# Performance work log

Measured on AMD Instinct MI355X. Metric: run time of the kernel, lower is better.

## Reference

```python
import jax, jax.numpy as jnp
import numpy as np

EMB = 1024
HEADS = 16
HEAD_DIM = EMB // HEADS


def setup_inputs() -> dict:
    key = jax.random.key(0)
    ks = jax.random.split(key, 5)
    x = jax.random.normal(ks[0], (2, 2048, EMB), dtype=jnp.float32)
    # per-head projection params, stacked over heads: [H, E, D]
    Wq = jax.random.normal(ks[1], (HEADS, EMB, HEAD_DIM), dtype=jnp.float32)
    Wk = jax.random.normal(ks[2], (HEADS, EMB, HEAD_DIM), dtype=jnp.float32)
    Wv = jax.random.normal(ks[3], (HEADS, EMB, HEAD_DIM), dtype=jnp.float32)
    # output projection (torch Linear weight [out, in], bias=False)
    Wo = jax.random.normal(ks[4], (EMB, EMB), dtype=jnp.float32) * (1.0 / np.sqrt(EMB))
    return {"x": x, "Wq": Wq, "Wk": Wk, "Wv": Wv, "Wo": Wo}


def reference(x, Wq, Wk, Wv, Wo):
    B, T, E = x.shape
    # per-head projections: [B, H, T, D]
    q = jnp.einsum('bte,hed->bhtd', x, Wq)
    k = jnp.einsum('bte,hed->bhtd', x, Wk)
    v = jnp.einsum('bte,hed->bhtd', x, Wv)
    scale = 1.0 / jnp.sqrt(jnp.asarray(HEAD_DIM, dtype=x.dtype))
    scores = jnp.einsum('bhtd,bhsd->bhts', q, k) * scale  # [B,H,T,T]
    s = jax.nn.softmax(scores, axis=-1)
    out = jnp.einsum('bhts,bhsd->bhtd', s, v)
    # concat heads along last dim in head order: [B, T, H*D]
    combined = jnp.transpose(out, (0, 2, 1, 3)).reshape(B, T, E)
    # residual + output projection (Linear bias=False: y = combined @ Wo.T)
    return x + combined @ Wo.T
```

## Files before the change

kernel.cpp:

```cpp
#include <hip/hip_runtime.h>

#define EMB   1024
#define HEADS 16
#define HDIM  64
#define BATCH 2
#define SEQ   2048
#define MROWS (BATCH*SEQ)
#define STR   40
#define QSCALE 0.1803368801111204f

typedef __attribute__((ext_vector_type(8))) short bf16x8;
typedef __attribute__((ext_vector_type(4))) float f32x4;
typedef unsigned short u16;

__device__ __forceinline__ u16 f2bf(float f) {
    unsigned u = __float_as_uint(f);
    u += 0x7fffu + ((u >> 16) & 1u);
    return (u16)(u >> 16);
}
__device__ __forceinline__ float bf2f(u16 h) {
    return __uint_as_float((unsigned)h << 16);
}
__device__ __forceinline__ float fast_exp2(float x) {
#if __has_builtin(__builtin_amdgcn_exp2f)
    return __builtin_amdgcn_exp2f(x);
#else
    return __expf(x * 0.6931471805599453f);
#endif
}
__device__ __forceinline__ unsigned pk_trunc(float lo, float hi) {
    return __builtin_amdgcn_perm(__float_as_uint(hi), __float_as_uint(lo),
                                 0x07060302u);
}

#define SWZ(r, ch) ((((r) << 6)) + ((((ch) ^ ((r) & 7))) << 3))

__global__ __launch_bounds__(256)
void prep1(const float* __restrict__ X, const float* __restrict__ Wq,
           const float* __restrict__ Wk, const float* __restrict__ Wv,
           u16* __restrict__ Xh, u16* __restrict__ Xl,
           u16* __restrict__ Qth, u16* __restrict__ Qtl,
           u16* __restrict__ Kth, u16* __restrict__ Ktl,
           u16* __restrict__ Vth)
{
    const int bx = blockIdx.x;
    if (bx < 2048) {
        int i = (bx * 256 + threadIdx.x) * 8;
#pragma unroll
        for (int half = 0; half < 2; ++half) {
            float4 v = *(const float4*)(X + i + half * 4);
            ushort4 hi, lo;
            hi.x = f2bf(v.x); lo.x = f2bf(v.x - bf2f(hi.x));
            hi.y = f2bf(v.y); lo.y = f2bf(v.y - bf2f(hi.y));
            hi.z = f2bf(v.z); lo.z = f2bf(v.z - bf2f(hi.z));
            hi.w = f2bf(v.w); lo.w = f2bf(v.w - bf2f(hi.w));
            *(ushort4*)(Xh + i + half * 4) = hi;
            *(ushort4*)(Xl + i + half * 4) = lo;
        }
    } else if (bx < 3072) {
        const int f = bx - 2048;
        const int z = f >> 9, y = (f >> 5) & 15, x = f & 31;
        const float* W  = z ? Wk  : Wq;
        u16* Oh         = z ? Kth : Qth;
        u16* Ol         = z ? Ktl : Qtl;
        const int d  = threadIdx.x & 63;
        const int e0 = (x * 4 + (threadIdx.x >> 6)) * 8;
        const float* src = W + ((size_t)y * EMB + e0) * HDIM + d;
        ushort4 h0, h1, l0, l1;
        float v; u16 hv;
        v = src[0 * 64]; hv = f2bf(v); h0.x = hv; l0.x = f2bf(v - bf2f(hv));
        v = src[1 * 64]; hv = f2bf(v); h0.y = hv; l0.y = f2bf(v - bf2f(hv));
        v = src[2 * 64]; hv = f2bf(v); h0.z = hv; l0.z = f2bf(v - bf2f(hv));
        v = src[3 * 64]; hv = f2bf(v); h0.w = hv; l0.w = f2bf(v - bf2f(hv));
        v = src[4 * 64]; hv = f2bf(v); h1.x = hv; l1.x = f2bf(v - bf2f(hv));
        v = src[5 * 64]; hv = f2bf(v); h1.y = hv; l1.y = f2bf(v - bf2f(hv));
        v = src[6 * 64]; hv = f2bf(v); h1.z = hv; l1.z = f2bf(v - bf2f(hv));
        v = src[7 * 64]; hv = f2bf(v); h1.w = hv; l1.w = f2bf(v - bf2f(hv));
        size_t obase = ((size_t)y * HDIM + d) * EMB + e0;
        *(ushort4*)(Oh + obase)     = h0;
        *(ushort4*)(Oh + obase + 4) = h1;
        *(ushort4*)(Ol + obase)     = l0;
        *(ushort4*)(Ol + obase + 4) = l1;
    } else {
        const int f = bx - 3072;
        const int y = f >> 5, x = f & 31;
        const int d  = threadIdx.x & 63;
        const int e0 = (x * 4 + (threadIdx.x >> 6)) * 8;
        const float* src = Wv + ((size_t)y * EMB + e0) * HDIM + d;
        ushort4 h0, h1;
        h0.x = f2bf(src[0 * 64]); h0.y = f2bf(src[1 * 64]);
        h0.z = f2bf(src[2 * 64]); h0.w = f2bf(src[3 * 64]);
        h1.x = f2bf(src[4 * 64]); h1.y = f2bf(src[5 * 64]);
        h1.z = f2bf(src[6 * 64]); h1.w = f2bf(src[7 * 64]);
        size_t obase = ((size_t)y * HDIM + d) * EMB + e0;
        *(ushort4*)(Vth + obase)     = h0;
        *(ushort4*)(Vth + obase + 4) = h1;
    }
}

__global__ __launch_bounds__(256, 2)
void qkv_fused(const u16* __restrict__ Xh, const u16* __restrict__ Xl,
               const u16* __restrict__ Wqh, const u16* __restrict__ Wql,
               const u16* __restrict__ Wkh, const u16* __restrict__ Wkl,
               const u16* __restrict__ Wvt,
               u16* __restrict__ Qh, u16* __restrict__ Ql,
               u16* __restrict__ Kh, u16* __restrict__ Kl,
               u16* __restrict__ Vt)
{
    const int z  = blockIdx.z;
    const bool isV = (z == 2);
    const int m0 = blockIdx.x * 128;
    const int n0 = blockIdx.y * 128;
    const int t    = threadIdx.x;
    const int wave = t >> 6, lane = t & 63;
    const int wm = wave & 1, wn = wave >> 1;
    const int l16 = lane & 15, quad = lane >> 4;

    __shared__ u16 Ahs[128][STR];
    __shared__ u16 Als[128][STR];
    __shared__ u16 Bhs[128][STR];
    __shared__ u16 Bls[128][STR];

    const u16* Bh_g = isV ? Wvt : (z ? Wkh : Wqh);
    const u16* Bl_g = z ? Wkl : Wql;

    const int ar0 = t >> 2, ak = (t & 3) * 8, ar1 = ar0 + 64;

    f32x4 acc[4][4];
#pragma unroll
    for (int i = 0; i < 4; ++i)
#pragma unroll
        for (int j = 0; j < 4; ++j) acc[i][j] = (f32x4){0.f, 0.f, 0.f, 0.f};

    bf16x8 cur[8], nxt[8], nx2[8];
#define QK_LOAD(dst, kk)                                                            \
    do {                                                                            \
        dst[0] = *(const bf16x8*)(Xh  + (size_t)(m0 + ar0) * EMB + (kk) + ak);      \
        dst[1] = *(const bf16x8*)(Xh  + (size_t)(m0 + ar1) * EMB + (kk) + ak);      \
        dst[4] = *(const bf16x8*)(Bh_g + (size_t)(n0 + ar0) * EMB + (kk) + ak);     \
        dst[5] = *(const bf16x8*)(Bh_g + (size_t)(n0 + ar1) * EMB + (kk) + ak);     \
        if (!isV) {                                                                 \
            dst[2] = *(const bf16x8*)(Xl  + (size_t)(m0 + ar0) * EMB + (kk) + ak);  \
            dst[3] = *(const bf16x8*)(Xl  + (size_t)(m0 + ar1) * EMB + (kk) + ak);  \
            dst[6] = *(const bf16x8*)(Bl_g + (size_t)(n0 + ar0) * EMB + (kk) + ak); \
            dst[7] = *(const bf16x8*)(Bl_g + (size_t)(n0 + ar1) * EMB + (kk) + ak); \
        }                                                                           \
    } while (0)

    QK_LOAD(cur, 0);
    QK_LOAD(nxt, 32);

    for (int k0 = 0; k0 < EMB; k0 += 32) {
        __syncthreads();
        *(bf16x8*)&Ahs[ar0][ak] = cur[0];  *(bf16x8*)&Ahs[ar1][ak] = cur[1];
        *(bf16x8*)&Bhs[ar0][ak] = cur[4];  *(bf16x8*)&Bhs[ar1][ak] = cur[5];
        if (!isV) {
            *(bf16x8*)&Als[ar0][ak] = cur[2];  *(bf16x8*)&Als[ar1][ak] = cur[3];
            *(bf16x8*)&Bls[ar0][ak] = cur[6];  *(bf16x8*)&Bls[ar1][ak] = cur[7];
        }
        __syncthreads();

        const int kn = (k0 + 64 < EMB) ? k0 + 64 : 0;
        QK_LOAD(nx2, kn);

        bf16x8 B4h[4], B4l[4];
#pragma unroll
        for (int j = 0; j < 4; ++j) {
            B4h[j] = *(const bf16x8*)&Bhs[wn * 64 + 16 * j + l16][quad * 8];
            if (!isV)
                B4l[j] = *(const bf16x8*)&Bls[wn * 64 + 16 * j + l16][quad * 8];
        }
#pragma unroll
        for (int i = 0; i < 4; ++i) {
            bf16x8 Ai_h = *(const bf16x8*)&Ahs[wm * 64 + 16 * i + l16][quad * 8];
            if (!isV) {
                bf16x8 Ai_l = *(const bf16x8*)&Als[wm * 64 + 16 * i + l16][quad * 8];
#pragma unroll
                for (int j = 0; j < 4; ++j) {
                    acc[i][j] = __builtin_amdgcn_mfma_f32_16x16x32_bf16(Ai_h, B4h[j], acc[i][j], 0, 0, 0);
                    acc[i][j] = __builtin_amdgcn_mfma_f32_16x16x32_bf16(Ai_h, B4l[j], acc[i][j], 0, 0, 0);
                    acc[i][j] = __builtin_amdgcn_mfma_f32_16x16x32_bf16(Ai_l, B4h[j], acc[i][j], 0, 0, 0);
                }
            } else {
#pragma unroll
                for (int j = 0; j < 4; ++j)
                    acc[i][j] = __builtin_amdgcn_mfma_f32_16x16x32_bf16(Ai_h, B4h[j], acc[i][j], 0, 0, 0);
            }
        }
#pragma unroll
        for (int q = 0; q < 8; ++q) { cur[q] = nxt[q]; nxt[q] = nx2[q]; }
    }
#undef QK_LOAD

    const int b = m0 >> 11;
    const int h = (n0 + wn * 64) >> 6;
    if (isV) {
#pragma unroll
        for (int i = 0; i < 4; ++i)
#pragma unroll
            for (int j = 0; j < 4; ++j) {
                int d  = 16 * j + l16;
                int tt = (m0 & (SEQ - 1)) + wm * 64 + 16 * i + quad * 4;
                ushort4 o;
                o.x = f2bf(acc[i][j][0]); o.y = f2bf(acc[i][j][1]);
                o.z = f2bf(acc[i][j][2]); o.w = f2bf(acc[i][j][3]);
                *(ushort4*)(Vt + ((size_t)(b * HEADS + h) * HDIM + d) * SEQ + tt) = o;
            }
    } else {
        u16* Oh = z ? Kh : Qh;
        u16* Ol = z ? Kl : Ql;
        const float esc = z ? 1.0f : QSCALE;
#pragma unroll
        for (int i = 0; i < 4; ++i)
#pragma unroll
            for (int r = 0; r < 4; ++r) {
                int tt = (m0 & (SEQ - 1)) + wm * 64 + 16 * i + quad * 4 + r;
                size_t rowbase = ((size_t)(b * HEADS + h) * SEQ + tt) * HDIM;
#pragma unroll
                for (int j = 0; j < 4; ++j) {
                    int d = 16 * j + l16;
                    float v = acc[i][j][r] * esc;
                    u16 hv = f2bf(v);
                    Oh[rowbase + d] = hv;
                    Ol[rowbase + d] = f2bf(v - bf2f(hv));
                }
            }
    }
}

__global__ __launch_bounds__(256, 4)
void attn_mfma(const u16* __restrict__ Qh, const u16* __restrict__ Ql,
               const u16* __restrict__ Kh, const u16* __restrict__ Kl,
               const u16* __restrict__ Vt, u16* __restrict__ Cb,
               const float* __restrict__ Wo, u16* __restrict__ Woh)
{
    const int w = blockIdx.x;
    if (w >= 1024) {
        int base = ((w - 1024) * 256 + threadIdx.x) * 8;
#pragma unroll 4
        for (int it = 0; it < 32; ++it) {
#pragma unroll
            for (int half = 0; half < 2; ++half) {
                float4 v = *(const float4*)(Wo + base + half * 4);
                ushort4 o;
                o.x = f2bf(v.x); o.y = f2bf(v.y); o.z = f2bf(v.z); o.w = f2bf(v.w);
                *(ushort4*)(Woh + base + half * 4) = o;
            }
            base += 16 * 256 * 8;
        }
        return;
    }

    const int g    = w >> 3;
    const int qt0  = (g & 31) * 64;
    const int bh   = (w & 7) + ((g >> 5) << 3);

    const int t    = threadIdx.x;
    const int wave = t >> 6;
    const int lane = t & 63;
    const int l16  = lane & 15;
    const int quad = lane >> 4;

    __shared__ u16 Ksh[4096];
    __shared__ u16 Ksl[4096];
    __shared__ u16 Vs [4096];
    __shared__ u16 Ps [4096];

    const size_t bh_off = (size_t)bh * SEQ * HDIM;
    const u16* Qhb = Qh + bh_off;
    const u16* Qlb = Ql + bh_off;
    const u16* Khb = Kh + bh_off;
    const u16* Klb = Kl + bh_off;
    const u16* Vtb = Vt + bh_off;

    const int qrow = qt0 + wave * 16 + l16;
    bf16x8 aQh[2], aQl[2];
    {
        const u16* bH = Qhb + (size_t)qrow * HDIM + quad * 8;
        const u16* bL = Qlb + (size_t)qrow * HDIM + quad * 8;
        aQh[0] = *(const bf16x8*)(bH);
        aQh[1] = *(const bf16x8*)(bH + 32);
        aQl[0] = *(const bf16x8*)(bL);
        aQl[1] = *(const bf16x8*)(bL + 32);
    }

    f32x4 accO[4];
    float m_i = -1e30f, l_i = 0.f;
#pragma unroll
    for (int j = 0; j < 4; ++j) accO[j] = (f32x4){0.f, 0.f, 0.f, 0.f};

    const int sr0 = t >> 3, sch = t & 7, sr1 = sr0 + 32;
    const int gc  = sch * 8;
    const int so0 = SWZ(sr0, sch), so1 = SWZ(sr1, sch);

    bf16x8 cur[6], nxt[6];
#define KV_LOAD(dst, ss)                                                       \
    do {                                                                       \
        dst[0] = *(const bf16x8*)(Khb + (size_t)((ss) + sr0) * HDIM + gc);     \
        dst[1] = *(const bf16x8*)(Khb + (size_t)((ss) + sr1) * HDIM + gc);     \
        dst[2] = *(const bf16x8*)(Klb + (size_t)((ss) + sr0) * HDIM + gc);     \
        dst[3] = *(const bf16x8*)(Klb + (size_t)((ss) + sr1) * HDIM + gc);     \
        dst[4] = *(const bf16x8*)(Vtb + (size_t)sr0 * SEQ + (ss) + gc);        \
        dst[5] = *(const bf16x8*)(Vtb + (size_t)sr1 * SEQ + (ss) + gc);        \
    } while (0)

    KV_LOAD(cur, 0);

    for (int s0 = 0; s0 < SEQ; s0 += 64) {
        __syncthreads();
        *(bf16x8*)&Ksh[so0] = cur[0];  *(bf16x8*)&Ksh[so1] = cur[1];
        *(bf16x8*)&Ksl[so0] = cur[2];  *(bf16x8*)&Ksl[so1] = cur[3];
        *(bf16x8*)&Vs [so0] = cur[4];  *(bf16x8*)&Vs [so1] = cur[5];
        __syncthreads();

        const int sn = (s0 + 64 < SEQ) ? s0 + 64 : 0;
        KV_LOAD(nxt, sn);

        f32x4 accS[4];
#pragma unroll
        for (int i = 0; i < 4; ++i) accS[i] = (f32x4){0.f, 0.f, 0.f, 0.f};
        __builtin_amdgcn_s_setprio(1);
#pragma unroll
        for (int c = 0; c < 2; ++c) {
#pragma unroll
            for (int i = 0; i < 4; ++i) {
                bf16x8 kh_ = *(const bf16x8*)&Ksh[SWZ(16 * i + l16, 4 * c + quad)];
                bf16x8 kl_ = *(const bf16x8*)&Ksl[SWZ(16 * i + l16, 4 * c + quad)];
                accS[i] = __builtin_amdgcn_mfma_f32_16x16x32_bf16(kh_, aQh[c], accS[i], 0, 0, 0);
                accS[i] = __builtin_amdgcn_mfma_f32_16x16x32_bf16(kl_, aQh[c], accS[i], 0, 0, 0);
                accS[i] = __builtin_amdgcn_mfma_f32_16x16x32_bf16(kh_, aQl[c], accS[i], 0, 0, 0);
            }
        }
        __builtin_amdgcn_s_setprio(0);

        {
            float vmax = fmaxf(fmaxf(accS[0][0], accS[0][1]),
                               fmaxf(accS[0][2], accS[0][3]));
#pragma unroll
            for (int i = 1; i < 4; ++i)
                vmax = fmaxf(vmax, fmaxf(fmaxf(accS[i][0], accS[i][1]),
                                         fmaxf(accS[i][2], accS[i][3])));
            vmax = fmaxf(vmax, __shfl_xor(vmax, 16, 64));
            vmax = fmaxf(vmax, __shfl_xor(vmax, 32, 64));
            float mn   = fmaxf(m_i, vmax);
            float alph = fast_exp2(m_i - mn);
            m_i = mn;
            float P[4][4], s = 0.f;
#pragma unroll
            for (int i = 0; i < 4; ++i)
#pragma unroll
                for (int r = 0; r < 4; ++r) {
                    P[i][r] = fast_exp2(accS[i][r] - mn);
                    s += P[i][r];
                }
            s += __shfl_xor(s, 16, 64);
            s += __shfl_xor(s, 32, 64);
            l_i = l_i * alph + s;
#pragma unroll
            for (int j = 0; j < 4; ++j) accO[j] *= alph;

            const int prow = wave * 16 + l16;
#pragma unroll
            for (int i = 0; i < 4; ++i) {
                uint2 pv;
                pv.x = pk_trunc(P[i][0], P[i][1]);
                pv.y = pk_trunc(P[i][2], P[i][3]);
                *(uint2*)&Ps[SWZ(prow, 2 * i + (quad >> 1)) + ((quad & 1) << 2)] = pv;
            }
        }

        __builtin_amdgcn_s_setprio(1);
#pragma unroll
        for (int c = 0; c < 2; ++c) {
            bf16x8 bP = *(const bf16x8*)&Ps[SWZ(wave * 16 + l16, 4 * c + quad)];
#pragma unroll
            for (int j = 0; j < 4; ++j) {
                bf16x8 aV = *(const bf16x8*)&Vs[SWZ(16 * j + l16, 4 * c + quad)];
                accO[j] = __builtin_amdgcn_mfma_f32_16x16x32_bf16(aV, bP, accO[j], 0, 0, 0);
            }
        }
        __builtin_amdgcn_s_setprio(0);
#pragma unroll
        for (int q = 0; q < 6; ++q) cur[q] = nxt[q];
    }
#undef KV_LOAD

    const int b = bh >> 4, h = bh & 15;
    {
        const int row = qt0 + wave * 16 + l16;
        const float inv = 1.f / l_i;
#pragma unroll
        for (int j = 0; j < 4; ++j) {
            ushort4 o;
            o.x = f2bf(accO[j][0] * inv); o.y = f2bf(accO[j][1] * inv);
            o.z = f2bf(accO[j][2] * inv); o.w = f2bf(accO[j][3] * inv);
            *(ushort4*)&Cb[((size_t)b * SEQ + row) * EMB + h * HDIM + 16 * j + quad * 4] = o;
        }
    }
}

__global__ __launch_bounds__(256, 2)
void oproj_mfma(const u16* __restrict__ Cb, const u16* __restrict__ Woh,
                const float* __restrict__ X, float* __restrict__ Y)
{
    const int m0 = blockIdx.x * 64;
    const int n0 = blockIdx.y * 128;
    const int t    = threadIdx.x;
    const int wave = t >> 6, lane = t & 63;
    const int wm = wave & 1, wn = wave >> 1;
    const int l16 = lane & 15, quad = lane >> 4;

    __shared__ u16 Ahs[64][STR];
    __shared__ u16 Bhs[128][STR];

    const int ar0 = t >> 2, ak = (t & 3) * 8, ar1 = ar0 + 64;

    f32x4 acc[2][4];
#pragma unroll
    for (int i = 0; i < 2; ++i)
#pragma unroll
        for (int j = 0; j < 4; ++j) acc[i][j] = (f32x4){0.f, 0.f, 0.f, 0.f};

    bf16x8 cur[3], nxt[3], nx2[3];
#define O_LOAD(dst, kk)                                                         \
    do {                                                                        \
        dst[0] = *(const bf16x8*)(Cb  + (size_t)(m0 + ar0) * EMB + (kk) + ak);  \
        dst[1] = *(const bf16x8*)(Woh + (size_t)(n0 + ar0) * EMB + (kk) + ak);  \
        dst[2] = *(const bf16x8*)(Woh + (size_t)(n0 + ar1) * EMB + (kk) + ak);  \
    } while (0)

    O_LOAD(cur, 0);
    O_LOAD(nxt, 32);

    for (int k0 = 0; k0 < EMB; k0 += 32) {
        __syncthreads();
        *(bf16x8*)&Ahs[ar0][ak] = cur[0];
        *(bf16x8*)&Bhs[ar0][ak] = cur[1];  *(bf16x8*)&Bhs[ar1][ak] = cur[2];
        __syncthreads();

        const int kn = (k0 + 64 < EMB) ? k0 + 64 : 0;
        O_LOAD(nx2, kn);

        bf16x8 B4[4];
#pragma unroll
        for (int j = 0; j < 4; ++j)
            B4[j] = *(const bf16x8*)&Bhs[wn * 64 + 16 * j + l16][quad * 8];
#pragma unroll
        for (int i = 0; i < 2; ++i) {
            bf16x8 Ai = *(const bf16x8*)&Ahs[wm * 32 + 16 * i + l16][quad * 8];
#pragma unroll
            for (int j = 0; j < 4; ++j)
                acc[i][j] = __builtin_amdgcn_mfma_f32_16x16x32_bf16(Ai, B4[j], acc[i][j], 0, 0, 0);
        }
#pragma unroll
        for (int q = 0; q < 3; ++q) { cur[q] = nxt[q]; nxt[q] = nx2[q]; }
    }
#undef O_LOAD

#pragma unroll
    for (int i = 0; i < 2; ++i)
#pragma unroll
        for (int r = 0; r < 4; ++r) {
            int m = m0 + wm * 32 + 16 * i + quad * 4 + r;
#pragma unroll
            for (int j = 0; j < 4; ++j) {
                int n = n0 + wn * 64 + 16 * j + l16;
                Y[(size_t)m * EMB + n] = acc[i][j][r] + X[(size_t)m * EMB + n];
            }
        }
}

extern "C" void kernel_launch(void* const* d_in, const int* in_sizes, int n_in,
                              void* d_out, int out_size, void* d_ws,
                              size_t ws_size, hipStream_t stream)
{
    const float* x  = (const float*)d_in[0];
    const float* Wq = (const float*)d_in[1];
    const float* Wk = (const float*)d_in[2];
    const float* Wv = (const float*)d_in[3];
    const float* Wo = (const float*)d_in[4];
    float* Y = (float*)d_out;

    const size_t NPER = (size_t)MROWS * EMB;
    u16* base  = (u16*)d_ws;
    u16* Qh    = base;
    u16* Ql    = Qh + NPER;
    u16* Kh    = Ql + NPER;
    u16* Kl    = Kh + NPER;
    u16* Vt    = Kl + NPER;
    u16* Xh    = Vt + NPER;
    u16* Xl    = Xh + NPER;
    u16* Wtq_h = Xl + NPER;
    u16* Wtq_l = Wtq_h + EMB * EMB;
    u16* Wtk_h = Wtq_l + EMB * EMB;
    u16* Wtk_l = Wtk_h + EMB * EMB;
    u16* Wvt   = (u16*)d_out;
    u16* Cb    = Xh;
    u16* Woh   = Xl;

    prep1<<<dim3(3584), 256, 0, stream>>>(x, Wq, Wk, Wv, Xh, Xl,
                                          Wtq_h, Wtq_l, Wtk_h, Wtk_l, Wvt);
    qkv_fused<<<dim3(32, 8, 3), 256, 0, stream>>>(Xh, Xl, Wtq_h, Wtq_l,
                                                  Wtk_h, Wtk_l, Wvt,
                                                  Qh, Ql, Kh, Kl, Vt);
    attn_mfma<<<dim3(1040), 256, 0, stream>>>(Qh, Ql, Kh, Kl, Vt, Cb, Wo, Woh);
    oproj_mfma<<<dim3(64, 8), 256, 0, stream>>>(Cb, Woh, x, Y);
}
```

Baseline: 268.9 us.

## Switch attention to 32x32x16 MFMA with 128-row query tiles and register-shuffled P

The attention kernel moves from 16x16x32 to 32x32x16 bf16 MFMA tiles. Each wave now owns 32 query rows and each block owns 128, which halves the grid and the K/V tile reloads per query. The probability matrix is passed from the score layout to the PV operand layout with cross-lane shuffles instead of an LDS round trip, so the Ps buffer goes away. The cost is more accumulator registers per lane, with launch bounds lowered to 2 blocks per SM, and only 512 attention blocks, which could reduce occupancy and hurt load balance.

```diff
diff --git a/kernel.cpp b/kernel.cpp
--- a/kernel.cpp
+++ b/kernel.cpp
@@ -11,6 +11,7 @@
 
 typedef __attribute__((ext_vector_type(8))) short bf16x8;
 typedef __attribute__((ext_vector_type(4))) float f32x4;
+typedef __attribute__((ext_vector_type(16))) float f32x16;
 typedef unsigned short u16;
 
 __device__ __forceinline__ u16 f2bf(float f) {
@@ -228,15 +229,15 @@
     }
 }
 
-__global__ __launch_bounds__(256, 4)
+__global__ __launch_bounds__(256, 2)
 void attn_mfma(const u16* __restrict__ Qh, const u16* __restrict__ Ql,
                const u16* __restrict__ Kh, const u16* __restrict__ Kl,
                const u16* __restrict__ Vt, u16* __restrict__ Cb,
                const float* __restrict__ Wo, u16* __restrict__ Woh)
 {
     const int w = blockIdx.x;
-    if (w >= 1024) {
-        int base = ((w - 1024) * 256 + threadIdx.x) * 8;
+    if (w >= 512) {
+        int base = ((w - 512) * 256 + threadIdx.x) * 8;
 #pragma unroll 4
         for (int it = 0; it < 32; ++it) {
 #pragma unroll
@@ -252,19 +253,18 @@
     }
 
     const int g    = w >> 3;
-    const int qt0  = (g & 31) * 64;
-    const int bh   = (w & 7) + ((g >> 5) << 3);
+    const int qt0  = (g & 15) * 128;
+    const int bh   = (w & 7) + ((g >> 4) << 3);
 
     const int t    = threadIdx.x;
     const int wave = t >> 6;
     const int lane = t & 63;
-    const int l16  = lane & 15;
-    const int quad = lane >> 4;
+    const int l31  = lane & 31;
+    const int hi   = lane >> 5;
 
     __shared__ u16 Ksh[4096];
     __shared__ u16 Ksl[4096];
     __shared__ u16 Vs [4096];
-    __shared__ u16 Ps [4096];
 
     const size_t bh_off = (size_t)bh * SEQ * HDIM;
     const u16* Qhb = Qh + bh_off;
@@ -273,21 +273,23 @@
     const u16* Klb = Kl + bh_off;
     const u16* Vtb = Vt + bh_off;
 
-    const int qrow = qt0 + wave * 16 + l16;
-    bf16x8 aQh[2], aQl[2];
-    {
-        const u16* bH = Qhb + (size_t)qrow * HDIM + quad * 8;
-        const u16* bL = Qlb + (size_t)qrow * HDIM + quad * 8;
-        aQh[0] = *(const bf16x8*)(bH);
-        aQh[1] = *(const bf16x8*)(bH + 32);
-        aQl[0] = *(const bf16x8*)(bL);
-        aQl[1] = *(const bf16x8*)(bL + 32);
-    }
-
-    f32x4 accO[4];
+    const int qw0 = qt0 + wave * 32;
+
+    bf16x8 bQh[4], bQl[4];
+#pragma unroll
+    for (int ks = 0; ks < 4; ++ks) {
+        const u16* pH = Qhb + (size_t)(qw0 + l31) * HDIM + ks * 16 + hi * 8;
+        const u16* pL = Qlb + (size_t)(qw0 + l31) * HDIM + ks * 16 + hi * 8;
+        bQh[ks] = *(const bf16x8*)pH;
+        bQl[ks] = *(const bf16x8*)pL;
+    }
+
+    f32x16 accO[2];
+#pragma unroll
+    for (int dt = 0; dt < 2; ++dt)
+#pragma unroll
+        for (int r = 0; r < 16; ++r) accO[dt][r] = 0.f;
     float m_i = -1e30f, l_i = 0.f;
-#pragma unroll
-    for (int j = 0; j < 4; ++j) accO[j] = (f32x4){0.f, 0.f, 0.f, 0.f};
 
     const int sr0 = t >> 3, sch = t & 7, sr1 = sr0 + 32;
     const int gc  = sch * 8;
@@ -316,68 +318,93 @@
         const int sn = (s0 + 64 < SEQ) ? s0 + 64 : 0;
         KV_LOAD(nxt, sn);
 
-        f32x4 accS[4];
-#pragma unroll
-        for (int i = 0; i < 4; ++i) accS[i] = (f32x4){0.f, 0.f, 0.f, 0.f};
+        f32x16 accS[2];
+#pragma unroll
+        for (int kt = 0; kt < 2; ++kt)
+#pragma unroll
+            for (int r = 0; r < 16; ++r) accS[kt][r] = 0.f;
         __builtin_amdgcn_s_setprio(1);
 #pragma unroll
-        for (int c = 0; c < 2; ++c) {
-#pragma unroll
-            for (int i = 0; i < 4; ++i) {
-                bf16x8 kh_ = *(const bf16x8*)&Ksh[SWZ(16 * i + l16, 4 * c + quad)];
-                bf16x8 kl_ = *(const bf16x8*)&Ksl[SWZ(16 * i + l16, 4 * c + quad)];
-                accS[i] = __builtin_amdgcn_mfma_f32_16x16x32_bf16(kh_, aQh[c], accS[i], 0, 0, 0);
-                accS[i] = __builtin_amdgcn_mfma_f32_16x16x32_bf16(kl_, aQh[c], accS[i], 0, 0, 0);
-                accS[i] = __builtin_amdgcn_mfma_f32_16x16x32_bf16(kh_, aQl[c], accS[i], 0, 0, 0);
-            }
+        for (int ks = 0; ks < 4; ++ks) {
+            bf16x8 kh0 = *(const bf16x8*)&Ksh[SWZ(l31,      2 * ks + hi)];
+            bf16x8 kh1 = *(const bf16x8*)&Ksh[SWZ(32 + l31, 2 * ks + hi)];
+            bf16x8 kl0 = *(const bf16x8*)&Ksl[SWZ(l31,      2 * ks + hi)];
+            bf16x8 kl1 = *(const bf16x8*)&Ksl[SWZ(32 + l31, 2 * ks + hi)];
+            accS[0] = __builtin_amdgcn_mfma_f32_32x32x16_bf16(kh0, bQh[ks], accS[0], 0, 0, 0);
+            accS[1] = __builtin_amdgcn_mfma_f32_32x32x16_bf16(kh1, bQh[ks], accS[1], 0, 0, 0);
+            accS[0] = __builtin_amdgcn_mfma_f32_32x32x16_bf16(kl0, bQh[ks], accS[0], 0, 0, 0);
+            accS[1] = __builtin_amdgcn_mfma_f32_32x32x16_bf16(kl1, bQh[ks], accS[1], 0, 0, 0);
+            accS[0] = __builtin_amdgcn_mfma_f32_32x32x16_bf16(kh0, bQl[ks], accS[0], 0, 0, 0);
+            accS[1] = __builtin_amdgcn_mfma_f32_32x32x16_bf16(kh1, bQl[ks], accS[1], 0, 0, 0);
         }
         __builtin_amdgcn_s_setprio(0);
 
+        float P[2][16];
         {
-            float vmax = fmaxf(fmaxf(accS[0][0], accS[0][1]),
-                               fmaxf(accS[0][2], accS[0][3]));
-#pragma unroll
-            for (int i = 1; i < 4; ++i)
-                vmax = fmaxf(vmax, fmaxf(fmaxf(accS[i][0], accS[i][1]),
-                                         fmaxf(accS[i][2], accS[i][3])));
-            vmax = fmaxf(vmax, __shfl_xor(vmax, 16, 64));
+            float vmax = accS[0][0];
+#pragma unroll
+            for (int r = 1; r < 16; ++r) vmax = fmaxf(vmax, accS[0][r]);
+#pragma unroll
+            for (int r = 0; r < 16; ++r) vmax = fmaxf(vmax, accS[1][r]);
             vmax = fmaxf(vmax, __shfl_xor(vmax, 32, 64));
             float mn   = fmaxf(m_i, vmax);
             float alph = fast_exp2(m_i - mn);
             m_i = mn;
-            float P[4][4], s = 0.f;
-#pragma unroll
-            for (int i = 0; i < 4; ++i)
-#pragma unroll
-                for (int r = 0; r < 4; ++r) {
-                    P[i][r] = fast_exp2(accS[i][r] - mn);
-                    s += P[i][r];
+            float s = 0.f;
+#pragma unroll
+            for (int kt = 0; kt < 2; ++kt)
+#pragma unroll
+                for (int r = 0; r < 16; ++r) {
+                    P[kt][r] = fast_exp2(accS[kt][r] - mn);
+                    s += P[kt][r];
                 }
-            s += __shfl_xor(s, 16, 64);
             s += __shfl_xor(s, 32, 64);
             l_i = l_i * alph + s;
 #pragma unroll
-            for (int j = 0; j < 4; ++j) accO[j] *= alph;
-
-            const int prow = wave * 16 + l16;
-#pragma unroll
-            for (int i = 0; i < 4; ++i) {
-                uint2 pv;
-                pv.x = pk_trunc(P[i][0], P[i][1]);
-                pv.y = pk_trunc(P[i][2], P[i][3]);
-                *(uint2*)&Ps[SWZ(prow, 2 * i + (quad >> 1)) + ((quad & 1) << 2)] = pv;
+            for (int dt = 0; dt < 2; ++dt)
+#pragma unroll
+                for (int r = 0; r < 16; ++r) accO[dt][r] *= alph;
+        }
+
+        unsigned pp[2][4][2];
+#pragma unroll
+        for (int kt = 0; kt < 2; ++kt)
+#pragma unroll
+            for (int rq = 0; rq < 4; ++rq) {
+                pp[kt][rq][0] = pk_trunc(P[kt][4 * rq + 0], P[kt][4 * rq + 1]);
+                pp[kt][rq][1] = pk_trunc(P[kt][4 * rq + 2], P[kt][4 * rq + 3]);
             }
+        unsigned rcv[2][2][2];
+#pragma unroll
+        for (int kt = 0; kt < 2; ++kt)
+#pragma unroll
+            for (int m = 0; m < 2; ++m)
+#pragma unroll
+                for (int u = 0; u < 2; ++u) {
+                    unsigned snd = hi ? pp[kt][2 * m][u] : pp[kt][2 * m + 1][u];
+                    rcv[kt][m][u] = __shfl_xor(snd, 32, 64);
+                }
+        bf16x8 bP[4];
+#pragma unroll
+        for (int ks = 0; ks < 4; ++ks) {
+            const int kt = ks >> 1, m = ks & 1;
+            unsigned a0 = pp[kt][2 * m + hi][0], a1 = pp[kt][2 * m + hi][1];
+            unsigned b0 = rcv[kt][m][0],         b1 = rcv[kt][m][1];
+            union { unsigned u[4]; bf16x8 v; } tmp;
+            tmp.u[0] = hi ? b0 : a0;
+            tmp.u[1] = hi ? b1 : a1;
+            tmp.u[2] = hi ? a0 : b0;
+            tmp.u[3] = hi ? a1 : b1;
+            bP[ks] = tmp.v;
         }
 
         __builtin_amdgcn_s_setprio(1);
 #pragma unroll
-        for (int c = 0; c < 2; ++c) {
-            bf16x8 bP = *(const bf16x8*)&Ps[SWZ(wave * 16 + l16, 4 * c + quad)];
-#pragma unroll
-            for (int j = 0; j < 4; ++j) {
-                bf16x8 aV = *(const bf16x8*)&Vs[SWZ(16 * j + l16, 4 * c + quad)];
-                accO[j] = __builtin_amdgcn_mfma_f32_16x16x32_bf16(aV, bP, accO[j], 0, 0, 0);
-            }
+        for (int ks = 0; ks < 4; ++ks) {
+            bf16x8 aV0 = *(const bf16x8*)&Vs[SWZ(l31,      2 * ks + hi)];
+            bf16x8 aV1 = *(const bf16x8*)&Vs[SWZ(32 + l31, 2 * ks + hi)];
+            accO[0] = __builtin_amdgcn_mfma_f32_32x32x16_bf16(aV0, bP[ks], accO[0], 0, 0, 0);
+            accO[1] = __builtin_amdgcn_mfma_f32_32x32x16_bf16(aV1, bP[ks], accO[1], 0, 0, 0);
         }
         __builtin_amdgcn_s_setprio(0);
 #pragma unroll
@@ -386,17 +413,21 @@
 #undef KV_LOAD
 
     const int b = bh >> 4, h = bh & 15;
-    {
-        const int row = qt0 + wave * 16 + l16;
-        const float inv = 1.f / l_i;
-#pragma unroll
-        for (int j = 0; j < 4; ++j) {
+    const int qrow = qw0 + l31;
+    const float inv = 1.f / l_i;
+    u16* crow = Cb + ((size_t)b * SEQ + qrow) * EMB + h * HDIM;
+#pragma unroll
+    for (int dt = 0; dt < 2; ++dt)
+#pragma unroll
+        for (int rq = 0; rq < 4; ++rq) {
+            const int d0 = dt * 32 + 8 * rq + 4 * hi;
             ushort4 o;
-            o.x = f2bf(accO[j][0] * inv); o.y = f2bf(accO[j][1] * inv);
-            o.z = f2bf(accO[j][2] * inv); o.w = f2bf(accO[j][3] * inv);
-            *(ushort4*)&Cb[((size_t)b * SEQ + row) * EMB + h * HDIM + 16 * j + quad * 4] = o;
-        }
-    }
+            o.x = f2bf(accO[dt][4 * rq + 0] * inv);
+            o.y = f2bf(accO[dt][4 * rq + 1] * inv);
+            o.z = f2bf(accO[dt][4 * rq + 2] * inv);
+            o.w = f2bf(accO[dt][4 * rq + 3] * inv);
+            *(ushort4*)(crow + d0) = o;
+        }
 }
 
 __global__ __launch_bounds__(256, 2)
@@ -503,6 +534,6 @@
     qkv_fused<<<dim3(32, 8, 3), 256, 0, stream>>>(Xh, Xl, Wtq_h, Wtq_l,
                                                   Wtk_h, Wtk_l, Wvt,
                                                   Qh, Ql, Kh, Kl, Vt);
-    attn_mfma<<<dim3(1040), 256, 0, stream>>>(Qh, Ql, Kh, Kl, Vt, Cb, Wo, Woh);
+    attn_mfma<<<dim3(528), 256, 0, stream>>>(Qh, Ql, Kh, Kl, Vt, Cb, Wo, Woh);
     oproj_mfma<<<dim3(64, 8), 256, 0, stream>>>(Cb, Woh, x, Y);
 }
```

New measurement: 277.7 us. 1.03x slower.

## Restructure attention to 32x32 MFMA with split-K waves and direct-to-LDS loads

Applied to the files above, without the earlier changes.

Rewrites the attention kernel to use 32x32x16 bf16 MFMAs. Waves are split into two query halves times two key halves, and the two key-half partial softmax states are merged through LDS at the end. K/V tiles are double-buffered via global_load_lds straight into LDS, with one barrier per iteration instead of two. The P matrix is passed between MFMAs through lane shuffles rather than LDS, and a lazy rescale skips the accumulator correction when the running max grows by at most 8. The larger LDS footprint lowers occupancy to 3 blocks, and the lazy-max threshold risks exp2 overflow margins.

```diff
diff --git a/kernel.cpp b/kernel.cpp
--- a/kernel.cpp
+++ b/kernel.cpp
@@ -11,6 +11,7 @@
 
 typedef __attribute__((ext_vector_type(8))) short bf16x8;
 typedef __attribute__((ext_vector_type(4))) float f32x4;
+typedef __attribute__((ext_vector_type(16))) float f32x16;
 typedef unsigned short u16;
 
 __device__ __forceinline__ u16 f2bf(float f) {
@@ -31,6 +32,11 @@
 __device__ __forceinline__ unsigned pk_trunc(float lo, float hi) {
     return __builtin_amdgcn_perm(__float_as_uint(hi), __float_as_uint(lo),
                                  0x07060302u);
+}
+__device__ __forceinline__ void gload16(const u16* g, u16* l) {
+    __builtin_amdgcn_global_load_lds(
+        (const __attribute__((address_space(1))) unsigned int*)g,
+        (__attribute__((address_space(3))) unsigned int*)l, 16, 0, 0);
 }
 
 #define SWZ(r, ch) ((((r) << 6)) + ((((ch) ^ ((r) & 7))) << 3))
@@ -228,7 +234,7 @@
     }
 }
 
-__global__ __launch_bounds__(256, 4)
+__global__ __launch_bounds__(256, 3)
 void attn_mfma(const u16* __restrict__ Qh, const u16* __restrict__ Ql,
                const u16* __restrict__ Kh, const u16* __restrict__ Kl,
                const u16* __restrict__ Vt, u16* __restrict__ Cb,
@@ -251,20 +257,19 @@
         return;
     }
 
-    const int g    = w >> 3;
-    const int qt0  = (g & 31) * 64;
-    const int bh   = (w & 7) + ((g >> 5) << 3);
+    const int g     = w >> 3;
+    const int qtile = g & 31;
+    const int bh    = (w & 7) + ((g >> 5) << 3);
 
     const int t    = threadIdx.x;
     const int wave = t >> 6;
     const int lane = t & 63;
-    const int l16  = lane & 15;
-    const int quad = lane >> 4;
-
-    __shared__ u16 Ksh[4096];
-    __shared__ u16 Ksl[4096];
-    __shared__ u16 Vs [4096];
-    __shared__ u16 Ps [4096];
+    const int l31  = lane & 31;
+    const int hi   = lane >> 5;
+    const int wq   = wave & 1;
+    const int wk   = wave >> 1;
+
+    __shared__ u16 lds[24576];
 
     const size_t bh_off = (size_t)bh * SEQ * HDIM;
     const u16* Qhb = Qh + bh_off;
@@ -273,128 +278,166 @@
     const u16* Klb = Kl + bh_off;
     const u16* Vtb = Vt + bh_off;
 
-    const int qrow = qt0 + wave * 16 + l16;
-    bf16x8 aQh[2], aQl[2];
-    {
-        const u16* bH = Qhb + (size_t)qrow * HDIM + quad * 8;
-        const u16* bL = Qlb + (size_t)qrow * HDIM + quad * 8;
-        aQh[0] = *(const bf16x8*)(bH);
-        aQh[1] = *(const bf16x8*)(bH + 32);
-        aQl[0] = *(const bf16x8*)(bL);
-        aQl[1] = *(const bf16x8*)(bL + 32);
-    }
-
-    f32x4 accO[4];
+    const int qb0 = qtile * 64 + wq * 32;
+
+    bf16x8 bQh[4], bQl[4];
+#pragma unroll
+    for (int ks = 0; ks < 4; ++ks) {
+        const u16* pH = Qhb + (size_t)(qb0 + l31) * HDIM + ks * 16 + hi * 8;
+        const u16* pL = Qlb + (size_t)(qb0 + l31) * HDIM + ks * 16 + hi * 8;
+        bQh[ks] = *(const bf16x8*)pH;
+        bQl[ks] = *(const bf16x8*)pL;
+    }
+
+    f32x16 accO0, accO1;
+#pragma unroll
+    for (int r = 0; r < 16; ++r) { accO0[r] = 0.f; accO1[r] = 0.f; }
     float m_i = -1e30f, l_i = 0.f;
-#pragma unroll
-    for (int j = 0; j < 4; ++j) accO[j] = (f32x4){0.f, 0.f, 0.f, 0.f};
-
-    const int sr0 = t >> 3, sch = t & 7, sr1 = sr0 + 32;
-    const int gc  = sch * 8;
-    const int so0 = SWZ(sr0, sch), so1 = SWZ(sr1, sch);
-
-    bf16x8 cur[6], nxt[6];
-#define KV_LOAD(dst, ss)                                                       \
-    do {                                                                       \
-        dst[0] = *(const bf16x8*)(Khb + (size_t)((ss) + sr0) * HDIM + gc);     \
-        dst[1] = *(const bf16x8*)(Khb + (size_t)((ss) + sr1) * HDIM + gc);     \
-        dst[2] = *(const bf16x8*)(Klb + (size_t)((ss) + sr0) * HDIM + gc);     \
-        dst[3] = *(const bf16x8*)(Klb + (size_t)((ss) + sr1) * HDIM + gc);     \
-        dst[4] = *(const bf16x8*)(Vtb + (size_t)sr0 * SEQ + (ss) + gc);        \
-        dst[5] = *(const bf16x8*)(Vtb + (size_t)sr1 * SEQ + (ss) + gc);        \
+
+    const int r8  = lane >> 3;
+    const int cSw = (lane & 7) ^ (r8 & 7);
+    const int rowA = wave * 16 + r8;
+    const size_t koffA = (size_t)rowA * HDIM + cSw * 8;
+    const size_t koffB = koffA + 8 * HDIM;
+    const size_t voffA = (size_t)rowA * SEQ + cSw * 8;
+    const size_t voffB = voffA + (size_t)8 * SEQ;
+
+#define STAGE(b, s0_)                                                              \
+    do { const int bb = (b) * 12288; const int wb = bb + wave * 1024;              \
+        gload16(Khb + (size_t)(s0_) * HDIM + koffA, &lds[wb]);                     \
+        gload16(Khb + (size_t)(s0_) * HDIM + koffB, &lds[wb + 512]);               \
+        gload16(Klb + (size_t)(s0_) * HDIM + koffA, &lds[wb + 4096]);              \
+        gload16(Klb + (size_t)(s0_) * HDIM + koffB, &lds[wb + 4096 + 512]);        \
+        gload16(Vtb + (s0_) + voffA,                &lds[wb + 8192]);              \
+        gload16(Vtb + (s0_) + voffB,                &lds[wb + 8192 + 512]);        \
     } while (0)
 
-    KV_LOAD(cur, 0);
-
-    for (int s0 = 0; s0 < SEQ; s0 += 64) {
+    STAGE(0, 0);
+    __syncthreads();
+
+    const int l7 = lane & 7;
+    for (int it = 0; it < 32; ++it) {
+        const int cur = it & 1;
+        if (it < 31) STAGE(cur ^ 1, (it + 1) * 64);
+
+        const u16* KhL = &lds[cur * 12288];
+        const u16* KlL = KhL + 4096;
+        const u16* VL  = KhL + 8192;
+
+        f32x16 accS;
+#pragma unroll
+        for (int r = 0; r < 16; ++r) accS[r] = 0.f;
+        __builtin_amdgcn_s_setprio(1);
+#pragma unroll
+        for (int ks = 0; ks < 4; ++ks) {
+            const int off = (wk * 32 + l31) * 64 + (((2 * ks + hi) ^ l7)) * 8;
+            bf16x8 kh = *(const bf16x8*)(KhL + off);
+            bf16x8 kl = *(const bf16x8*)(KlL + off);
+            accS = __builtin_amdgcn_mfma_f32_32x32x16_bf16(kh, bQh[ks], accS, 0, 0, 0);
+            accS = __builtin_amdgcn_mfma_f32_32x32x16_bf16(kl, bQh[ks], accS, 0, 0, 0);
+            accS = __builtin_amdgcn_mfma_f32_32x32x16_bf16(kh, bQl[ks], accS, 0, 0, 0);
+        }
+        __builtin_amdgcn_s_setprio(0);
+
+        float P[16];
+        {
+            float vmax = fmaxf(fmaxf(accS[0], accS[1]), fmaxf(accS[2], accS[3]));
+#pragma unroll
+            for (int r = 4; r < 16; r += 4)
+                vmax = fmaxf(vmax, fmaxf(fmaxf(accS[r], accS[r + 1]),
+                                         fmaxf(accS[r + 2], accS[r + 3])));
+            vmax = fmaxf(vmax, __shfl_xor(vmax, 32, 64));
+            if (!__all(vmax - m_i <= 8.0f)) {
+                float mn = fmaxf(m_i, vmax);
+                float alph = fast_exp2(m_i - mn);
+                m_i = mn;
+                l_i *= alph;
+#pragma unroll
+                for (int r = 0; r < 16; ++r) { accO0[r] *= alph; accO1[r] *= alph; }
+            }
+            float s = 0.f;
+#pragma unroll
+            for (int r = 0; r < 16; ++r) {
+                P[r] = fast_exp2(accS[r] - m_i);
+                s += P[r];
+            }
+            s += __shfl_xor(s, 32, 64);
+            l_i += s;
+        }
+
+        unsigned A_[4], B_[4];
+#pragma unroll
+        for (int rq = 0; rq < 4; ++rq) {
+            A_[rq] = pk_trunc(P[4 * rq + 0], P[4 * rq + 1]);
+            B_[rq] = pk_trunc(P[4 * rq + 2], P[4 * rq + 3]);
+        }
+        bf16x8 bP[2];
+#pragma unroll
+        for (int ks = 0; ks < 2; ++ks) {
+            unsigned sndA = hi ? A_[2 * ks] : A_[2 * ks + 1];
+            unsigned sndB = hi ? B_[2 * ks] : B_[2 * ks + 1];
+            unsigned rcvA = __shfl_xor(sndA, 32, 64);
+            unsigned rcvB = __shfl_xor(sndB, 32, 64);
+            union { unsigned u[4]; bf16x8 v; } tmp;
+            tmp.u[0] = hi ? rcvA : A_[2 * ks];
+            tmp.u[1] = hi ? rcvB : B_[2 * ks];
+            tmp.u[2] = hi ? A_[2 * ks + 1] : rcvA;
+            tmp.u[3] = hi ? B_[2 * ks + 1] : rcvB;
+            bP[ks] = tmp.v;
+        }
+
+        __builtin_amdgcn_s_setprio(1);
+#pragma unroll
+        for (int ks = 0; ks < 2; ++ks) {
+            const int c0 = (4 * wk + 2 * ks + hi);
+            bf16x8 v0 = *(const bf16x8*)(VL + l31 * 64        + ((c0 ^ l7)) * 8);
+            bf16x8 v1 = *(const bf16x8*)(VL + (32 + l31) * 64 + ((c0 ^ l7)) * 8);
+            accO0 = __builtin_amdgcn_mfma_f32_32x32x16_bf16(v0, bP[ks], accO0, 0, 0, 0);
+            accO1 = __builtin_amdgcn_mfma_f32_32x32x16_bf16(v1, bP[ks], accO1, 0, 0, 0);
+        }
+        __builtin_amdgcn_s_setprio(0);
+
         __syncthreads();
-        *(bf16x8*)&Ksh[so0] = cur[0];  *(bf16x8*)&Ksh[so1] = cur[1];
-        *(bf16x8*)&Ksl[so0] = cur[2];  *(bf16x8*)&Ksl[so1] = cur[3];
-        *(bf16x8*)&Vs [so0] = cur[4];  *(bf16x8*)&Vs [so1] = cur[5];
-        __syncthreads();
-
-        const int sn = (s0 + 64 < SEQ) ? s0 + 64 : 0;
-        KV_LOAD(nxt, sn);
-
-        f32x4 accS[4];
-#pragma unroll
-        for (int i = 0; i < 4; ++i) accS[i] = (f32x4){0.f, 0.f, 0.f, 0.f};
-        __builtin_amdgcn_s_setprio(1);
-#pragma unroll
-        for (int c = 0; c < 2; ++c) {
-#pragma unroll
-            for (int i = 0; i < 4; ++i) {
-                bf16x8 kh_ = *(const bf16x8*)&Ksh[SWZ(16 * i + l16, 4 * c + quad)];
-                bf16x8 kl_ = *(const bf16x8*)&Ksl[SWZ(16 * i + l16, 4 * c + quad)];
-                accS[i] = __builtin_amdgcn_mfma_f32_16x16x32_bf16(kh_, aQh[c], accS[i], 0, 0, 0);
-                accS[i] = __builtin_amdgcn_mfma_f32_16x16x32_bf16(kl_, aQh[c], accS[i], 0, 0, 0);
-                accS[i] = __builtin_amdgcn_mfma_f32_16x16x32_bf16(kh_, aQl[c], accS[i], 0, 0, 0);
-            }
-        }
-        __builtin_amdgcn_s_setprio(0);
-
-        {
-            float vmax = fmaxf(fmaxf(accS[0][0], accS[0][1]),
-                               fmaxf(accS[0][2], accS[0][3]));
-#pragma unroll
-            for (int i = 1; i < 4; ++i)
-                vmax = fmaxf(vmax, fmaxf(fmaxf(accS[i][0], accS[i][1]),
-                                         fmaxf(accS[i][2], accS[i][3])));
-            vmax = fmaxf(vmax, __shfl_xor(vmax, 16, 64));
-            vmax = fmaxf(vmax, __shfl_xor(vmax, 32, 64));
-            float mn   = fmaxf(m_i, vmax);
-            float alph = fast_exp2(m_i - mn);
-            m_i = mn;
-            float P[4][4], s = 0.f;
-#pragma unroll
-            for (int i = 0; i < 4; ++i)
-#pragma unroll
-                for (int r = 0; r < 4; ++r) {
-                    P[i][r] = fast_exp2(accS[i][r] - mn);
-                    s += P[i][r];
-                }
-            s += __shfl_xor(s, 16, 64);
-            s += __shfl_xor(s, 32, 64);
-            l_i = l_i * alph + s;
-#pragma unroll
-            for (int j = 0; j < 4; ++j) accO[j] *= alph;
-
-            const int prow = wave * 16 + l16;
-#pragma unroll
-            for (int i = 0; i < 4; ++i) {
-                uint2 pv;
-                pv.x = pk_trunc(P[i][0], P[i][1]);
-                pv.y = pk_trunc(P[i][2], P[i][3]);
-                *(uint2*)&Ps[SWZ(prow, 2 * i + (quad >> 1)) + ((quad & 1) << 2)] = pv;
-            }
-        }
-
-        __builtin_amdgcn_s_setprio(1);
-#pragma unroll
-        for (int c = 0; c < 2; ++c) {
-            bf16x8 bP = *(const bf16x8*)&Ps[SWZ(wave * 16 + l16, 4 * c + quad)];
-#pragma unroll
-            for (int j = 0; j < 4; ++j) {
-                bf16x8 aV = *(const bf16x8*)&Vs[SWZ(16 * j + l16, 4 * c + quad)];
-                accO[j] = __builtin_amdgcn_mfma_f32_16x16x32_bf16(aV, bP, accO[j], 0, 0, 0);
-            }
-        }
-        __builtin_amdgcn_s_setprio(0);
-#pragma unroll
-        for (int q = 0; q < 6; ++q) cur[q] = nxt[q];
-    }
-#undef KV_LOAD
-
-    const int b = bh >> 4, h = bh & 15;
-    {
-        const int row = qt0 + wave * 16 + l16;
-        const float inv = 1.f / l_i;
-#pragma unroll
-        for (int j = 0; j < 4; ++j) {
+    }
+#undef STAGE
+
+    float* fb = (float*)lds;
+    const int slot = (wave * 64 + lane) * 34;
+#pragma unroll
+    for (int r = 0; r < 16; ++r) {
+        fb[slot + r]      = accO0[r];
+        fb[slot + 16 + r] = accO1[r];
+    }
+    fb[slot + 32] = m_i;
+    fb[slot + 33] = l_i;
+    __syncthreads();
+    if (wk == 0) {
+        const int ps = ((wave + 2) * 64 + lane) * 34;
+        const float m1 = fb[ps + 32], l1 = fb[ps + 33];
+        const float mS = fmaxf(m_i, m1);
+        float f0 = fast_exp2(m_i - mS);
+        float f1 = fast_exp2(m1 - mS);
+        const float inv = 1.f / (l_i * f0 + l1 * f1);
+        f0 *= inv; f1 *= inv;
+        const int b = bh >> 4, h = bh & 15;
+        u16* crow = Cb + ((size_t)b * SEQ + qb0 + l31) * EMB + h * HDIM;
+#pragma unroll
+        for (int rq = 0; rq < 4; ++rq) {
             ushort4 o;
-            o.x = f2bf(accO[j][0] * inv); o.y = f2bf(accO[j][1] * inv);
-            o.z = f2bf(accO[j][2] * inv); o.w = f2bf(accO[j][3] * inv);
-            *(ushort4*)&Cb[((size_t)b * SEQ + row) * EMB + h * HDIM + 16 * j + quad * 4] = o;
+            o.x = f2bf(accO0[4 * rq + 0] * f0 + fb[ps + 4 * rq + 0] * f1);
+            o.y = f2bf(accO0[4 * rq + 1] * f0 + fb[ps + 4 * rq + 1] * f1);
+            o.z = f2bf(accO0[4 * rq + 2] * f0 + fb[ps + 4 * rq + 2] * f1);
+            o.w = f2bf(accO0[4 * rq + 3] * f0 + fb[ps + 4 * rq + 3] * f1);
+            *(ushort4*)(crow + 8 * rq + 4 * hi) = o;
+        }
+#pragma unroll
+        for (int rq = 0; rq < 4; ++rq) {
+            ushort4 o;
+            o.x = f2bf(accO1[4 * rq + 0] * f0 + fb[ps + 16 + 4 * rq + 0] * f1);
+            o.y = f2bf(accO1[4 * rq + 1] * f0 + fb[ps + 16 + 4 * rq + 1] * f1);
+            o.z = f2bf(accO1[4 * rq + 2] * f0 + fb[ps + 16 + 4 * rq + 2] * f1);
+            o.w = f2bf(accO1[4 * rq + 3] * f0 + fb[ps + 16 + 4 * rq + 3] * f1);
+            *(ushort4*)(crow + 32 + 8 * rq + 4 * hi) = o;
         }
     }
 }
```

Result: slower. 282.2 us (+5.0%).

## Stage QKV GEMM tiles with direct global-to-LDS loads and double buffering

Applied to the files above, without the earlier changes.

The QKV projection GEMM stops staging tiles through registers. Tiles now go straight into a double-buffered LDS array with global_load_lds, and the two barriers per k-step become one. This frees the VGPRs that held the three prefetch stages and removes the LDS write instructions. In exchange the rows are unpadded (stride 32, no swizzle), so the MFMA fragment reads may hit LDS bank conflicts, and prefetch depth drops from two steps to one.

```diff
diff --git a/kernel.cpp b/kernel.cpp
--- a/kernel.cpp
+++ b/kernel.cpp
@@ -31,6 +31,11 @@
 __device__ __forceinline__ unsigned pk_trunc(float lo, float hi) {
     return __builtin_amdgcn_perm(__float_as_uint(hi), __float_as_uint(lo),
                                  0x07060302u);
+}
+__device__ __forceinline__ void gload16(const u16* g, u16* l) {
+    __builtin_amdgcn_global_load_lds(
+        (const __attribute__((address_space(1))) unsigned int*)g,
+        (__attribute__((address_space(3))) unsigned int*)l, 16, 0, 0);
 }
 
 #define SWZ(r, ch) ((((r) << 6)) + ((((ch) ^ ((r) & 7))) << 3))
@@ -116,15 +121,13 @@
     const int wm = wave & 1, wn = wave >> 1;
     const int l16 = lane & 15, quad = lane >> 4;
 
-    __shared__ u16 Ahs[128][STR];
-    __shared__ u16 Als[128][STR];
-    __shared__ u16 Bhs[128][STR];
-    __shared__ u16 Bls[128][STR];
+    __shared__ u16 lds[2 * 4 * 4096];
 
     const u16* Bh_g = isV ? Wvt : (z ? Wkh : Wqh);
     const u16* Bl_g = z ? Wkl : Wql;
 
-    const int ar0 = t >> 2, ak = (t & 3) * 8, ar1 = ar0 + 64;
+    const int srow = wave * 32 + (lane >> 2);
+    const int scol = (lane & 3) * 8;
 
     f32x4 acc[4][4];
 #pragma unroll
@@ -132,49 +135,43 @@
 #pragma unroll
         for (int j = 0; j < 4; ++j) acc[i][j] = (f32x4){0.f, 0.f, 0.f, 0.f};
 
-    bf16x8 cur[8], nxt[8], nx2[8];
-#define QK_LOAD(dst, kk)                                                            \
-    do {                                                                            \
-        dst[0] = *(const bf16x8*)(Xh  + (size_t)(m0 + ar0) * EMB + (kk) + ak);      \
-        dst[1] = *(const bf16x8*)(Xh  + (size_t)(m0 + ar1) * EMB + (kk) + ak);      \
-        dst[4] = *(const bf16x8*)(Bh_g + (size_t)(n0 + ar0) * EMB + (kk) + ak);     \
-        dst[5] = *(const bf16x8*)(Bh_g + (size_t)(n0 + ar1) * EMB + (kk) + ak);     \
-        if (!isV) {                                                                 \
-            dst[2] = *(const bf16x8*)(Xl  + (size_t)(m0 + ar0) * EMB + (kk) + ak);  \
-            dst[3] = *(const bf16x8*)(Xl  + (size_t)(m0 + ar1) * EMB + (kk) + ak);  \
-            dst[6] = *(const bf16x8*)(Bl_g + (size_t)(n0 + ar0) * EMB + (kk) + ak); \
-            dst[7] = *(const bf16x8*)(Bl_g + (size_t)(n0 + ar1) * EMB + (kk) + ak); \
-        }                                                                           \
+#define STAGE(buf, kk)                                                             \
+    do {                                                                           \
+        u16* Lb = &lds[(buf) * 16384];                                             \
+        u16* Ld0 = Lb + (wave * 32) * 32;                                          \
+        u16* Ld1 = Lb + (wave * 32 + 16) * 32;                                     \
+        gload16(Xh   + (size_t)(m0 + srow) * EMB + (kk) + scol,      Ld0);         \
+        gload16(Xh   + (size_t)(m0 + srow + 16) * EMB + (kk) + scol, Ld1);         \
+        gload16(Bh_g + (size_t)(n0 + srow) * EMB + (kk) + scol,      Ld0 + 8192);  \
+        gload16(Bh_g + (size_t)(n0 + srow + 16) * EMB + (kk) + scol, Ld1 + 8192);  \
+        if (!isV) {                                                                \
+            gload16(Xl   + (size_t)(m0 + srow) * EMB + (kk) + scol,      Ld0 + 4096); \
+            gload16(Xl   + (size_t)(m0 + srow + 16) * EMB + (kk) + scol, Ld1 + 4096); \
+            gload16(Bl_g + (size_t)(n0 + srow) * EMB + (kk) + scol,      Ld0 + 12288); \
+            gload16(Bl_g + (size_t)(n0 + srow + 16) * EMB + (kk) + scol, Ld1 + 12288); \
+        }                                                                          \
     } while (0)
 
-    QK_LOAD(cur, 0);
-    QK_LOAD(nxt, 32);
+    STAGE(0, 0);
+    __syncthreads();
 
     for (int k0 = 0; k0 < EMB; k0 += 32) {
-        __syncthreads();
-        *(bf16x8*)&Ahs[ar0][ak] = cur[0];  *(bf16x8*)&Ahs[ar1][ak] = cur[1];
-        *(bf16x8*)&Bhs[ar0][ak] = cur[4];  *(bf16x8*)&Bhs[ar1][ak] = cur[5];
-        if (!isV) {
-            *(bf16x8*)&Als[ar0][ak] = cur[2];  *(bf16x8*)&Als[ar1][ak] = cur[3];
-            *(bf16x8*)&Bls[ar0][ak] = cur[6];  *(bf16x8*)&Bls[ar1][ak] = cur[7];
-        }
-        __syncthreads();
-
-        const int kn = (k0 + 64 < EMB) ? k0 + 64 : 0;
-        QK_LOAD(nx2, kn);
-
+        const int cur = (k0 >> 5) & 1;
+        if (k0 + 32 < EMB) STAGE(cur ^ 1, k0 + 32);
+
+        const u16* Lb = &lds[cur * 16384];
         bf16x8 B4h[4], B4l[4];
 #pragma unroll
         for (int j = 0; j < 4; ++j) {
-            B4h[j] = *(const bf16x8*)&Bhs[wn * 64 + 16 * j + l16][quad * 8];
+            B4h[j] = *(const bf16x8*)(Lb + 8192 + (wn * 64 + 16 * j + l16) * 32 + quad * 8);
             if (!isV)
-                B4l[j] = *(const bf16x8*)&Bls[wn * 64 + 16 * j + l16][quad * 8];
+                B4l[j] = *(const bf16x8*)(Lb + 12288 + (wn * 64 + 16 * j + l16) * 32 + quad * 8);
         }
 #pragma unroll
         for (int i = 0; i < 4; ++i) {
-            bf16x8 Ai_h = *(const bf16x8*)&Ahs[wm * 64 + 16 * i + l16][quad * 8];
+            bf16x8 Ai_h = *(const bf16x8*)(Lb + (wm * 64 + 16 * i + l16) * 32 + quad * 8);
             if (!isV) {
-                bf16x8 Ai_l = *(const bf16x8*)&Als[wm * 64 + 16 * i + l16][quad * 8];
+                bf16x8 Ai_l = *(const bf16x8*)(Lb + 4096 + (wm * 64 + 16 * i + l16) * 32 + quad * 8);
 #pragma unroll
                 for (int j = 0; j < 4; ++j) {
                     acc[i][j] = __builtin_amdgcn_mfma_f32_16x16x32_bf16(Ai_h, B4h[j], acc[i][j], 0, 0, 0);
@@ -187,10 +184,9 @@
                     acc[i][j] = __builtin_amdgcn_mfma_f32_16x16x32_bf16(Ai_h, B4h[j], acc[i][j], 0, 0, 0);
             }
         }
-#pragma unroll
-        for (int q = 0; q < 8; ++q) { cur[q] = nxt[q]; nxt[q] = nx2[q]; }
-    }
-#undef QK_LOAD
+        __syncthreads();
+    }
+#undef STAGE
 
     const int b = m0 >> 11;
     const int h = (n0 + wn * 64) >> 6;
```

Result: faster. 254.9 us, median of 2 (-5.2%).
